# Performance work log

Hardware: AMD Instinct MI355X
Metric: run time of the kernel (lower is better)

Reference implementation:

```python
import jax, jax.numpy as jnp
import numpy as np

NUM_TAGS = 48
B, S = 512, 2048


def setup_inputs() -> dict:
    key = jax.random.key(0)
    k1, k2, k3, k4, k5 = jax.random.split(key, 5)
    emissions = jax.random.normal(k1, (B, S, NUM_TAGS), dtype=jnp.float32)
    tags = jax.random.randint(k2, (B, S), 0, NUM_TAGS, dtype=jnp.int32)
    mask = jnp.ones((B, S), dtype=jnp.float32)
    transitions = jax.random.uniform(k3, (NUM_TAGS, NUM_TAGS), minval=-0.1, maxval=0.1, dtype=jnp.float32)
    start_transitions = jax.random.uniform(k4, (NUM_TAGS,), minval=-0.1, maxval=0.1, dtype=jnp.float32)
    end_transitions = jax.random.uniform(k5, (NUM_TAGS,), minval=-0.1, maxval=0.1, dtype=jnp.float32)
    return {"emissions": emissions, "transitions": transitions,
            "start_transitions": start_transitions, "end_transitions": end_transitions,
            "tags": tags, "mask": mask}


def reference(emissions, transitions, start_transitions, end_transitions, tags, mask):
    # emissions: [B,S,T], tags: [B,S] int, mask: [B,S] float (1 = valid)
    b, s, t = emissions.shape
    barange = jnp.arange(b)

    # ---- gold path score (fully vectorized over time) ----
    emit = jnp.take_along_axis(emissions, tags[:, :, None], axis=2)[..., 0]  # [B,S]
    score = start_transitions[tags[:, 0]] + emit[:, 0]
    trans = transitions[tags[:, :-1], tags[:, 1:]]                            # [B,S-1]
    score = score + jnp.sum((trans + emit[:, 1:]) * mask[:, 1:], axis=1)
    last_idx = mask.sum(axis=1).astype(jnp.int32) - 1
    last_tags = tags[barange, last_idx]
    score = score + end_transitions[last_tags]

    # ---- log-partition via forward algorithm (scan over time) ----
    alpha0 = start_transitions[None, :] + emissions[:, 0]                     # [B,T]

    def step(alpha, xs):
        emit_t, mask_t = xs                                                   # [B,T], [B]
        # scores[b,i,j] = alpha[b,i] + transitions[i,j] + emit_t[b,j]
        scores = alpha[:, :, None] + transitions[None, :, :] + emit_t[:, None, :]
        next_alpha = jax.nn.logsumexp(scores, axis=1)                         # [B,T]
        m = mask_t[:, None]
        alpha = next_alpha * m + alpha * (1.0 - m)
        return alpha, None

    xs = (jnp.swapaxes(emissions[:, 1:], 0, 1), jnp.swapaxes(mask[:, 1:], 0, 1))
    alpha, _ = jax.lax.scan(step, alpha0, xs)
    partition = jax.nn.logsumexp(alpha + end_transitions[None, :], axis=1)    # [B]

    return -jnp.mean(score - partition)
```

## Files before the change

### kernel.cpp

```cpp
#include <hip/hip_runtime.h>

#define NTAGS 48
#define NB    512
#define SLEN  2048

typedef float f32x2 __attribute__((ext_vector_type(2)));


__device__ __forceinline__ float rl_f(float v, int l) {
  return __builtin_bit_cast(float, __builtin_amdgcn_readlane(__builtin_bit_cast(int, v), l));
}

template <int CTRL, bool BC>
__device__ __forceinline__ float dpp_mv(float oldv, float v) {
  return __builtin_bit_cast(float, __builtin_amdgcn_update_dpp(
      __builtin_bit_cast(int, oldv), __builtin_bit_cast(int, v), CTRL, 0xF, 0xF, BC));
}

__device__ __forceinline__ float wred_max(float v) {
  v = fmaxf(v, dpp_mv<0x128, false>(v, v));
  v = fmaxf(v, dpp_mv<0x124, false>(v, v));
  v = fmaxf(v, dpp_mv<0x122, false>(v, v));
  v = fmaxf(v, dpp_mv<0x121, false>(v, v));
  v = fmaxf(v, dpp_mv<0x142, false>(v, v));
  v = fmaxf(v, dpp_mv<0x143, false>(v, v));
  return rl_f(v, 63);
}

__device__ __forceinline__ float wred_sum(float v) {
  v += dpp_mv<0x128, true>(0.0f, v);
  v += dpp_mv<0x124, true>(0.0f, v);
  v += dpp_mv<0x122, true>(0.0f, v);
  v += dpp_mv<0x121, true>(0.0f, v);
  v += dpp_mv<0x142, true>(0.0f, v);
  v += dpp_mv<0x143, true>(0.0f, v);
  return rl_f(v, 63);
}

#define DOT4(L0, L1, L2, L3, E01, E23, SA, SB, SC, SD, PA, PB)              \
  asm("v_readlane_b32 " SA ", %2, " #L0 "\n\t"                              \
      "v_readlane_b32 " SB ", %2, " #L1 "\n\t"                              \
      "v_readlane_b32 " SC ", %2, " #L2 "\n\t"                              \
      "v_readlane_b32 " SD ", %2, " #L3 "\n\t"                              \
      "v_pk_fma_f32 %0, " PA ", %3, %0\n\t"                                 \
      "v_pk_fma_f32 %1, " PB ", %4, %1"                                     \
      : "+v"(a01), "+v"(a23)                                                \
      : "v"(pv), "v"(E01), "v"(E23)                                         \
      : "s80", "s81", "s82", "s83", "s84", "s85", "s86", "s87")

__device__ __forceinline__ float pkdot48(float pval, const f32x2* Ev2) {
  const int pv = __builtin_bit_cast(int, pval);
  f32x2 a01 = {0.0f, 0.0f};
  f32x2 a23 = {0.0f, 0.0f};
  DOT4(0, 1, 2, 3,     Ev2[0],  Ev2[1],  "s80","s81","s82","s83","s[80:81]","s[82:83]");
  DOT4(4, 5, 6, 7,     Ev2[2],  Ev2[3],  "s84","s85","s86","s87","s[84:85]","s[86:87]");
  DOT4(8, 9, 10, 11,   Ev2[4],  Ev2[5],  "s80","s81","s82","s83","s[80:81]","s[82:83]");
  DOT4(12, 13, 14, 15, Ev2[6],  Ev2[7],  "s84","s85","s86","s87","s[84:85]","s[86:87]");
  DOT4(16, 17, 18, 19, Ev2[8],  Ev2[9],  "s80","s81","s82","s83","s[80:81]","s[82:83]");
  DOT4(20, 21, 22, 23, Ev2[10], Ev2[11], "s84","s85","s86","s87","s[84:85]","s[86:87]");
  DOT4(24, 25, 26, 27, Ev2[12], Ev2[13], "s80","s81","s82","s83","s[80:81]","s[82:83]");
  DOT4(28, 29, 30, 31, Ev2[14], Ev2[15], "s84","s85","s86","s87","s[84:85]","s[86:87]");
  DOT4(32, 33, 34, 35, Ev2[16], Ev2[17], "s80","s81","s82","s83","s[80:81]","s[82:83]");
  DOT4(36, 37, 38, 39, Ev2[18], Ev2[19], "s84","s85","s86","s87","s[84:85]","s[86:87]");
  DOT4(40, 41, 42, 43, Ev2[20], Ev2[21], "s80","s81","s82","s83","s[80:81]","s[82:83]");
  DOT4(44, 45, 46, 47, Ev2[22], Ev2[23], "s84","s85","s86","s87","s[84:85]","s[86:87]");
  return (a01.x + a01.y) + (a23.x + a23.y);
}

__device__ __forceinline__ void renorm(float& p, float& cl) {
  float mx = wred_max(p);
  int e = ((__builtin_bit_cast(int, mx) >> 23) & 255) - 127;
  float r = __builtin_bit_cast(float, (127 - e) << 23);
  p *= r;
  cl += (float)e * 0.6931471805599453f;
}


extern "C" __global__ __launch_bounds__(64, 1)
void crf_main(const float* __restrict__ emis,
              const float* __restrict__ trans,
              const float* __restrict__ startt,
              const float* __restrict__ endt,
              const int*   __restrict__ tags,
              const float* __restrict__ mask,
              float* __restrict__ wa, float* __restrict__ wb,
              float* __restrict__ wsc, int* __restrict__ wcnt) {
  __shared__ float st[NTAGS * NTAGS];
  const int lane = threadIdx.x;
  const int bid  = blockIdx.x;

  if (bid >= 2 * NB) {
    const int b = bid - 2 * NB;
    for (int k = lane; k < NTAGS * NTAGS; k += 64) st[k] = trans[k];
    __syncthreads();
    const int* tb = tags + (size_t)b * SLEN;
    float ssum = 0.0f, csum = 0.0f;
    for (int it = 0; it < SLEN / 64; ++it) {
      const int t   = it * 64 + lane;
      int   cur = tb[t];
      float mv  = mask[(size_t)b * SLEN + t];
      float ev  = emis[((size_t)b * SLEN + t) * NTAGS + cur];
      float s;
      if (t == 0) {
        s = startt[cur] + ev;
      } else {
        int prev = tb[t - 1];
        s = (mv != 0.0f) ? (st[prev * NTAGS + cur] + ev) : 0.0f;
      }
      ssum += s;
      csum += (mv != 0.0f) ? 1.0f : 0.0f;
    }
    ssum = wred_sum(ssum);
    csum = wred_sum(csum);
    if (lane == 0) { wsc[b] = ssum; wcnt[b] = (int)(csum + 0.5f); }
    return;
  }

  const int  b   = bid >> 1;
  const bool fwd = (bid & 1) == 0;
  const int  jc  = lane < NTAGS ? lane : (NTAGS - 1);

  const float* eb = emis + (size_t)b * SLEN * NTAGS;
  const float* mb = mask + (size_t)b * SLEN;

  f32x2 Ev2[24];
  if (fwd) {
#pragma unroll
    for (int i = 0; i < NTAGS; i += 2) {
      Ev2[i / 2].x = __expf(trans[(i + 0) * NTAGS + jc]);
      Ev2[i / 2].y = __expf(trans[(i + 1) * NTAGS + jc]);
    }
  } else {
#pragma unroll
    for (int j = 0; j < NTAGS; j += 2) {
      Ev2[j / 2].x = __expf(trans[jc * NTAGS + j + 0]);
      Ev2[j / 2].y = __expf(trans[jc * NTAGS + j + 1]);
    }
  }

  float ebuf[8];
  float p, cl, een;

  if (fwd) {
    float mnext = mb[1 + (lane & 7)];
    float a0 = startt[jc] + eb[jc];
    if (lane >= NTAGS) a0 = -1e30f;
    float m0 = wred_max(a0);
    p  = __expf(a0 - m0);
    cl = m0;
#pragma unroll
    for (int k = 1; k <= 8; ++k) ebuf[k & 7] = eb[(size_t)k * NTAGS + jc];
    een = __expf(ebuf[1]);

    for (int g = 0; g < 128; ++g) {
      const int t0 = 1 + 8 * g;
      const uint32_t m8 = (uint32_t)__ballot(mnext != 0.0f) & 0xffu;
      mnext = mb[(size_t)(t0 + 8) + (lane & 7)];
      if (m8 == 0xffu) {
#pragma unroll
        for (int u = 0; u < 8; ++u) {
          const int t = t0 + u;
          float ee = een;
          een = __expf(ebuf[(t + 1) & 7]);
          float acc = pkdot48(p, Ev2);
          p = acc * ee;
          ebuf[t & 7] = eb[(size_t)(t + 8) * NTAGS + jc];
          if (u == 7) renorm(p, cl);
        }
      } else {
#pragma unroll
        for (int u = 0; u < 8; ++u) {
          const int t = t0 + u;
          float ee = een;
          een = __expf(ebuf[(t + 1) & 7]);
          float acc = pkdot48(p, Ev2);
          float pn  = acc * ee;
          p = ((m8 >> u) & 1u) ? pn : p;
          ebuf[t & 7] = eb[(size_t)(t + 8) * NTAGS + jc];
          if (u == 7) renorm(p, cl);
        }
      }
    }
    if (lane < NTAGS) wa[b * NTAGS + lane] = __logf(p) + cl;
  } else {
    float mnext = mb[2040 - (lane & 7)];
    float b0 = endt[jc];
    if (lane >= NTAGS) b0 = -1e30f;
    float m0 = wred_max(b0);
    p  = __expf(b0 - m0);
    cl = m0;
#pragma unroll
    for (int k = 0; k < 8; ++k) ebuf[(2047 - k) & 7] = eb[(size_t)(2047 - k) * NTAGS + jc];
    float q = p * __expf(ebuf[7]);
    een = __expf(ebuf[6]);

#pragma unroll
    for (int pt = 0; pt < 7; ++pt) {
      const int t = 2047 - pt;
      float ee = een;
      een = __expf(ebuf[(t + 6) & 7]);
      float acc = pkdot48(q, Ev2);
      float mv  = mb[t];
      p = (mv != 0.0f) ? acc : p;
      ebuf[t & 7] = eb[(size_t)(t - 8) * NTAGS + jc];
      if (pt == 6) renorm(p, cl);
      q = p * ee;
    }
    for (int g = 0; g < 127; ++g) {
      const int t0 = 2040 - 8 * g;
      const uint32_t m8 = (uint32_t)__ballot(mnext != 0.0f) & 0xffu;
      mnext = mb[(size_t)(t0 - 8) - (lane & 7)];
      if (m8 == 0xffu) {
#pragma unroll
        for (int u = 0; u < 8; ++u) {
          const int t = t0 - u;
          float ee = een;
          een = __expf(ebuf[(t + 6) & 7]);
          float acc = pkdot48(q, Ev2);
          p = acc;
          ebuf[t & 7] = eb[(size_t)(t - 8) * NTAGS + jc];
          if (u == 7) renorm(p, cl);
          q = p * ee;
        }
      } else {
#pragma unroll
        for (int u = 0; u < 8; ++u) {
          const int t = t0 - u;
          float ee = een;
          een = __expf(ebuf[(t + 6) & 7]);
          float acc = pkdot48(q, Ev2);
          p = ((m8 >> u) & 1u) ? acc : p;
          ebuf[t & 7] = eb[(size_t)(t - 8) * NTAGS + jc];
          if (u == 7) renorm(p, cl);
          q = p * ee;
        }
      }
    }
    if (lane < NTAGS) wb[b * NTAGS + lane] = __logf(p) + cl;
  }
}


extern "C" __global__ __launch_bounds__(64)
void crf_combine(const float* __restrict__ wa, const float* __restrict__ wb,
                 const float* __restrict__ wsc, const int* __restrict__ wcnt,
                 const int* __restrict__ tags, const float* __restrict__ endt,
                 float* __restrict__ out) {
  const int b    = blockIdx.x;
  const int lane = threadIdx.x;
  float v = -1e30f;
  if (lane < NTAGS) v = wa[b * NTAGS + lane] + wb[b * NTAGS + lane];
  float m = wred_max(v);
  float s = wred_sum(__expf(v - m));
  float part = m + __logf(s);
  int   last = wcnt[b] - 1;
  float score = wsc[b] + endt[tags[(size_t)b * SLEN + last]];
  if (lane == 0) atomicAdd(out, (part - score) * (1.0f / (float)NB));
}


extern "C" void kernel_launch(void* const* d_in, const int* in_sizes, int n_in,
                              void* d_out, int out_size, void* d_ws, size_t ws_size,
                              hipStream_t stream) {
  const float* emis  = (const float*)d_in[0];
  const float* trans = (const float*)d_in[1];
  const float* stt   = (const float*)d_in[2];
  const float* ent   = (const float*)d_in[3];
  const int*   tags  = (const int*)d_in[4];
  const float* mask  = (const float*)d_in[5];

  float* wa   = (float*)d_ws;
  float* wb   = wa + NB * NTAGS;
  float* wsc  = wb + NB * NTAGS;
  int*   wcnt = (int*)(wsc + NB);

  hipMemsetAsync(d_out, 0, sizeof(float), stream);
  crf_main<<<2 * NB + NB, 64, 0, stream>>>(emis, trans, stt, ent, tags, mask,
                                           wa, wb, wsc, wcnt);
  crf_combine<<<NB, 64, 0, stream>>>(wa, wb, wsc, wcnt, tags, ent, (float*)d_out);
}
```

Before: 421.3 us.

## Replace readlane dot product with DPP rotation and bpermute matvec; single-block combine

The per-step 48x48 matvec no longer broadcasts each lane's value through scalar readlanes with packed FMAs. It now rotates the probability vector within 16-lane rows using DPP row_ror, gets the other rows via three ds_bpermute ops, and uses a permuted per-lane transition table. The aim is to remove the 48 serial readlanes from the recurrence's critical path, at the cost of bpermute LDS latency and 48 scalar FMAs instead of 24 packed ones. The combine kernel becomes one 512-thread block with a shared-memory reduction and a plain store, dropping the memset and atomics.

```diff
diff --git a/kernel.cpp b/kernel.cpp
--- a/kernel.cpp
+++ b/kernel.cpp
@@ -3,8 +3,6 @@
 #define NTAGS 48
 #define NB    512
 #define SLEN  2048
-
-typedef float f32x2 __attribute__((ext_vector_type(2)));
 
 
 __device__ __forceinline__ float rl_f(float v, int l) {
@@ -37,34 +35,37 @@
   return rl_f(v, 63);
 }
 
-#define DOT4(L0, L1, L2, L3, E01, E23, SA, SB, SC, SD, PA, PB)              \
-  asm("v_readlane_b32 " SA ", %2, " #L0 "\n\t"                              \
-      "v_readlane_b32 " SB ", %2, " #L1 "\n\t"                              \
-      "v_readlane_b32 " SC ", %2, " #L2 "\n\t"                              \
-      "v_readlane_b32 " SD ", %2, " #L3 "\n\t"                              \
-      "v_pk_fma_f32 %0, " PA ", %3, %0\n\t"                                 \
-      "v_pk_fma_f32 %1, " PB ", %4, %1"                                     \
-      : "+v"(a01), "+v"(a23)                                                \
-      : "v"(pv), "v"(E01), "v"(E23)                                         \
-      : "s80", "s81", "s82", "s83", "s84", "s85", "s86", "s87")
-
-__device__ __forceinline__ float pkdot48(float pval, const f32x2* Ev2) {
-  const int pv = __builtin_bit_cast(int, pval);
-  f32x2 a01 = {0.0f, 0.0f};
-  f32x2 a23 = {0.0f, 0.0f};
-  DOT4(0, 1, 2, 3,     Ev2[0],  Ev2[1],  "s80","s81","s82","s83","s[80:81]","s[82:83]");
-  DOT4(4, 5, 6, 7,     Ev2[2],  Ev2[3],  "s84","s85","s86","s87","s[84:85]","s[86:87]");
-  DOT4(8, 9, 10, 11,   Ev2[4],  Ev2[5],  "s80","s81","s82","s83","s[80:81]","s[82:83]");
-  DOT4(12, 13, 14, 15, Ev2[6],  Ev2[7],  "s84","s85","s86","s87","s[84:85]","s[86:87]");
-  DOT4(16, 17, 18, 19, Ev2[8],  Ev2[9],  "s80","s81","s82","s83","s[80:81]","s[82:83]");
-  DOT4(20, 21, 22, 23, Ev2[10], Ev2[11], "s84","s85","s86","s87","s[84:85]","s[86:87]");
-  DOT4(24, 25, 26, 27, Ev2[12], Ev2[13], "s80","s81","s82","s83","s[80:81]","s[82:83]");
-  DOT4(28, 29, 30, 31, Ev2[14], Ev2[15], "s84","s85","s86","s87","s[84:85]","s[86:87]");
-  DOT4(32, 33, 34, 35, Ev2[16], Ev2[17], "s80","s81","s82","s83","s[80:81]","s[82:83]");
-  DOT4(36, 37, 38, 39, Ev2[18], Ev2[19], "s84","s85","s86","s87","s[84:85]","s[86:87]");
-  DOT4(40, 41, 42, 43, Ev2[20], Ev2[21], "s80","s81","s82","s83","s[80:81]","s[82:83]");
-  DOT4(44, 45, 46, 47, Ev2[22], Ev2[23], "s84","s85","s86","s87","s[84:85]","s[86:87]");
-  return (a01.x + a01.y) + (a23.x + a23.y);
+__device__ __forceinline__ float ror1(float v) {
+  return dpp_mv<0x121, false>(v, v);
+}
+
+__device__ __forceinline__ float rotdot48(float p, const float* Evp,
+                                          int a16, int a32, int a48,
+                                          bool isr2, bool isr0) {
+  const int pi = __builtin_bit_cast(int, p);
+  const float Bf = __builtin_bit_cast(float, __builtin_amdgcn_ds_bpermute(a16, pi));
+  const float Cf = __builtin_bit_cast(float, __builtin_amdgcn_ds_bpermute(a32, pi));
+  const float Df = __builtin_bit_cast(float, __builtin_amdgcn_ds_bpermute(a48, pi));
+  float a0 = 0.f, a1 = 0.f, a2 = 0.f, a3 = 0.f, a4 = 0.f, a5 = 0.f;
+  float s = p;
+#pragma unroll
+  for (int k = 0; k < 16; ++k) {
+    if (k & 1) a1 = fmaf(s, Evp[k], a1); else a0 = fmaf(s, Evp[k], a0);
+    if (k < 15) s = ror1(s);
+  }
+  float t = isr2 ? Cf : Bf;
+#pragma unroll
+  for (int k = 0; k < 16; ++k) {
+    if (k & 1) a3 = fmaf(t, Evp[16 + k], a3); else a2 = fmaf(t, Evp[16 + k], a2);
+    if (k < 15) t = ror1(t);
+  }
+  float u = isr0 ? Cf : Df;
+#pragma unroll
+  for (int k = 0; k < 16; ++k) {
+    if (k & 1) a5 = fmaf(u, Evp[32 + k], a5); else a4 = fmaf(u, Evp[32 + k], a4);
+    if (k < 15) u = ror1(u);
+  }
+  return ((a0 + a1) + (a2 + a3)) + (a4 + a5);
 }
 
 __device__ __forceinline__ void renorm(float& p, float& cl) {
@@ -118,23 +119,31 @@
 
   const int  b   = bid >> 1;
   const bool fwd = (bid & 1) == 0;
+  const int  r   = lane >> 4, c = lane & 15;
+  const bool isr2 = (r == 2), isr0 = (r == 0);
+  const int  a16 = (lane ^ 16) << 2;
+  const int  a32 = (lane ^ 32) << 2;
+  const int  a48 = (lane ^ 48) << 2;
   const int  jc  = lane < NTAGS ? lane : (NTAGS - 1);
 
   const float* eb = emis + (size_t)b * SLEN * NTAGS;
   const float* mb = mask + (size_t)b * SLEN;
 
-  f32x2 Ev2[24];
-  if (fwd) {
-#pragma unroll
-    for (int i = 0; i < NTAGS; i += 2) {
-      Ev2[i / 2].x = __expf(trans[(i + 0) * NTAGS + jc]);
-      Ev2[i / 2].y = __expf(trans[(i + 1) * NTAGS + jc]);
-    }
-  } else {
-#pragma unroll
-    for (int j = 0; j < NTAGS; j += 2) {
-      Ev2[j / 2].x = __expf(trans[jc * NTAGS + j + 0]);
-      Ev2[j / 2].y = __expf(trans[jc * NTAGS + j + 1]);
+  float Evp[48];
+  {
+    const int d0 = r;
+    const int d1 = isr2 ? 0 : (r ^ 1);
+    const int d2 = isr0 ? 2 : (r ^ 3);
+    const int drs[3] = {d0, d1, d2};
+#pragma unroll
+    for (int ph = 0; ph < 3; ++ph) {
+#pragma unroll
+      for (int k = 0; k < 16; ++k) {
+        int i = 16 * drs[ph] + ((c + k) & 15);
+        if (i > 47) i = 47;
+        Evp[ph * 16 + k] = __expf(fwd ? trans[i * NTAGS + jc]
+                                      : trans[jc * NTAGS + i]);
+      }
     }
   }
 
@@ -162,7 +171,7 @@
           const int t = t0 + u;
           float ee = een;
           een = __expf(ebuf[(t + 1) & 7]);
-          float acc = pkdot48(p, Ev2);
+          float acc = rotdot48(p, Evp, a16, a32, a48, isr2, isr0);
           p = acc * ee;
           ebuf[t & 7] = eb[(size_t)(t + 8) * NTAGS + jc];
           if (u == 7) renorm(p, cl);
@@ -173,7 +182,7 @@
           const int t = t0 + u;
           float ee = een;
           een = __expf(ebuf[(t + 1) & 7]);
-          float acc = pkdot48(p, Ev2);
+          float acc = rotdot48(p, Evp, a16, a32, a48, isr2, isr0);
           float pn  = acc * ee;
           p = ((m8 >> u) & 1u) ? pn : p;
           ebuf[t & 7] = eb[(size_t)(t + 8) * NTAGS + jc];
@@ -199,7 +208,7 @@
       const int t = 2047 - pt;
       float ee = een;
       een = __expf(ebuf[(t + 6) & 7]);
-      float acc = pkdot48(q, Ev2);
+      float acc = rotdot48(q, Evp, a16, a32, a48, isr2, isr0);
       float mv  = mb[t];
       p = (mv != 0.0f) ? acc : p;
       ebuf[t & 7] = eb[(size_t)(t - 8) * NTAGS + jc];
@@ -216,7 +225,7 @@
           const int t = t0 - u;
           float ee = een;
           een = __expf(ebuf[(t + 6) & 7]);
-          float acc = pkdot48(q, Ev2);
+          float acc = rotdot48(q, Evp, a16, a32, a48, isr2, isr0);
           p = acc;
           ebuf[t & 7] = eb[(size_t)(t - 8) * NTAGS + jc];
           if (u == 7) renorm(p, cl);
@@ -228,7 +237,7 @@
           const int t = t0 - u;
           float ee = een;
           een = __expf(ebuf[(t + 6) & 7]);
-          float acc = pkdot48(q, Ev2);
+          float acc = rotdot48(q, Evp, a16, a32, a48, isr2, isr0);
           p = ((m8 >> u) & 1u) ? acc : p;
           ebuf[t & 7] = eb[(size_t)(t - 8) * NTAGS + jc];
           if (u == 7) renorm(p, cl);
@@ -241,21 +250,36 @@
 }
 
 
-extern "C" __global__ __launch_bounds__(64)
+extern "C" __global__ __launch_bounds__(512)
 void crf_combine(const float* __restrict__ wa, const float* __restrict__ wb,
                  const float* __restrict__ wsc, const int* __restrict__ wcnt,
                  const int* __restrict__ tags, const float* __restrict__ endt,
                  float* __restrict__ out) {
-  const int b    = blockIdx.x;
-  const int lane = threadIdx.x;
-  float v = -1e30f;
-  if (lane < NTAGS) v = wa[b * NTAGS + lane] + wb[b * NTAGS + lane];
-  float m = wred_max(v);
-  float s = wred_sum(__expf(v - m));
+  __shared__ float red[8];
+  const int b = threadIdx.x;
+  float vv[NTAGS];
+  float m = -1e30f;
+#pragma unroll
+  for (int j = 0; j < NTAGS; ++j) {
+    vv[j] = wa[b * NTAGS + j] + wb[b * NTAGS + j];
+    m = fmaxf(m, vv[j]);
+  }
+  float s = 0.0f;
+#pragma unroll
+  for (int j = 0; j < NTAGS; ++j) s += __expf(vv[j] - m);
   float part = m + __logf(s);
-  int   last = wcnt[b] - 1;
-  float score = wsc[b] + endt[tags[(size_t)b * SLEN + last]];
-  if (lane == 0) atomicAdd(out, (part - score) * (1.0f / (float)NB));
+  const int   last  = wcnt[b] - 1;
+  const float score = wsc[b] + endt[tags[(size_t)b * SLEN + last]];
+  float val = (part - score) * (1.0f / (float)NB);
+  float wsum = wred_sum(val);
+  if ((b & 63) == 0) red[b >> 6] = wsum;
+  __syncthreads();
+  if (b == 0) {
+    float t = 0.0f;
+#pragma unroll
+    for (int w = 0; w < 8; ++w) t += red[w];
+    *out = t;
+  }
 }
 
 
@@ -274,8 +298,7 @@
   float* wsc  = wb + NB * NTAGS;
   int*   wcnt = (int*)(wsc + NB);
 
-  hipMemsetAsync(d_out, 0, sizeof(float), stream);
   crf_main<<<2 * NB + NB, 64, 0, stream>>>(emis, trans, stt, ent, tags, mask,
                                            wa, wb, wsc, wcnt);
-  crf_combine<<<NB, 64, 0, stream>>>(wa, wb, wsc, wcnt, tags, ent, (float*)d_out);
-}
+  crf_combine<<<1, 512, 0, stream>>>(wa, wb, wsc, wcnt, tags, ent, (float*)d_out);
+}
```

After: 552.9 us. 1.31x slower.
